# Kernel optimization log

Hardware: AMD Instinct MI355X
Metric: run time of the kernel (lower is better)

## Reference

```python
import jax, jax.numpy as jnp
import numpy as np

B, IN_DIM, D, C = 16384, 1024, 256, 100


def setup_inputs() -> dict:
    key = jax.random.key(0)
    k1, k2, k3, k4 = jax.random.split(key, 4)
    x = jax.random.normal(k1, (B, IN_DIM), dtype=jnp.float32)
    W = jax.random.normal(k2, (IN_DIM, D), dtype=jnp.float32) * (1.0 / np.sqrt(IN_DIM))
    b = jax.random.normal(k3, (D,), dtype=jnp.float32) * 0.01
    P = jax.random.normal(k4, (C, D), dtype=jnp.float32)  # class prototypes [C, D]
    return {"x": x, "W": W, "b": b, "P": P}


def reference(x, W, b, P):
    # Encoder: Z = x @ W + b  -> [B, D]
    Z = x @ W + b
    d = Z.shape[-1]
    # MSE(r, p) = mean((r - p)^2) = (|r|^2 - 2 r.p + |p|^2) / D
    # Computed via expansion to avoid the [B, C, D] broadcast intermediate.
    sq = (
        jnp.sum(Z * Z, axis=-1, keepdims=True)      # [B, 1]
        - 2.0 * (Z @ P.T)                            # [B, C]
        + jnp.sum(P * P, axis=-1)[None, :]           # [1, C]
    )
    return -sq / d  # [B, C]
```

## Files before the change

kernel.cpp:

```cpp
#include <hip/hip_runtime.h>

#define BATCH 16384
#define KDIM  1024
#define DDIM  256
#define CNUM  100
#define CPAD  112

typedef __bf16 bf16x8 __attribute__((ext_vector_type(8)));
typedef float  floatx4 __attribute__((ext_vector_type(4)));

static __device__ __forceinline__ unsigned short f2b(float f) {
    return __builtin_bit_cast(unsigned short, (__bf16)f);
}

__global__ __launch_bounds__(256) void prep(const float* __restrict__ W,
                                            const float* __restrict__ P,
                                            unsigned short* __restrict__ Wt2,
                                            unsigned short* __restrict__ Pbf,
                                            float* __restrict__ pnorm2) {
    __shared__ float T[32][33];
    const int bid = blockIdx.x;
    if (bid < 256) {
        const int k0 = (bid & 31) * 32;
        const int n0 = (bid >> 5) * 32;
        const int j  = threadIdx.x & 31;
        const int i0 = threadIdx.x >> 5;
#pragma unroll
        for (int l = 0; l < 4; ++l) {
            int i = i0 + l * 8;
            T[i][j] = W[(k0 + i) * DDIM + n0 + j];
        }
        __syncthreads();
        if (threadIdx.x < 128) {
            const int l  = threadIdx.x & 63;
            const int fn = threadIdx.x >> 6;
            const int lm = l & 15, lq = l >> 4;
            bf16x8 v;
#pragma unroll
            for (int jj = 0; jj < 8; ++jj)
                v[jj] = (__bf16)T[lq * 8 + jj][fn * 16 + lm];
            const int nblk = (n0 >> 4) + fn;
            const int kblk = k0 >> 5;
            *(bf16x8*)&Wt2[(nblk * 32 + kblk) * 512 + l * 8] = v;
        }
    } else {
        const int wave = threadIdx.x >> 6;
        const int lane = threadIdx.x & 63;
        const int c = (bid - 256) * 4 + wave;
        float s = 0.f;
#pragma unroll
        for (int jj = 0; jj < 4; ++jj) {
            int d = jj * 64 + lane;
            float v = (c < CNUM) ? P[c * DDIM + d] : 0.f;
            Pbf[c * DDIM + d] = f2b(v);
            s += v * v;
        }
#pragma unroll
        for (int m = 1; m < 64; m <<= 1) s += __shfl_xor(s, m, 64);
        if (lane == 0) pnorm2[c] = s;
    }
}

#define KSTEP(KK, CUR, NXT, P0, P1, P2, P3)                                    \
    {                                                                          \
        unsigned short* As_c = U + (CUR) * 4096;                               \
        const int kb_ = (KK) >> 5;                                             \
        if ((KK) + 64 < KDIM) {                                                \
            _Pragma("unroll")                                                  \
            for (int kf = 0; kf < 2; ++kf) {                                   \
                _Pragma("unroll")                                              \
                for (int f = 0; f < 4; ++f)                                    \
                    b[NXT][kf][f] = *(const bf16x8*)(gB + f * 16384 +          \
                                                     (kb_ + 2 + kf) * 512);    \
            }                                                                  \
            bf16x8 ha;                                                         \
            ha[0] = (__bf16)P0[0]; ha[1] = (__bf16)P0[1];                      \
            ha[2] = (__bf16)P0[2]; ha[3] = (__bf16)P0[3];                      \
            ha[4] = (__bf16)P1[0]; ha[5] = (__bf16)P1[1];                      \
            ha[6] = (__bf16)P1[2]; ha[7] = (__bf16)P1[3];                      \
            *(bf16x8*)&(U + (NXT) * 4096)[ldsA] = ha;                          \
            bf16x8 hb;                                                         \
            hb[0] = (__bf16)P2[0]; hb[1] = (__bf16)P2[1];                      \
            hb[2] = (__bf16)P2[2]; hb[3] = (__bf16)P2[3];                      \
            hb[4] = (__bf16)P3[0]; hb[5] = (__bf16)P3[1];                      \
            hb[6] = (__bf16)P3[2]; hb[7] = (__bf16)P3[3];                      \
            *(bf16x8*)&(U + (NXT) * 4096)[ldsA + 2048] = hb;                   \
            if ((KK) + 192 < KDIM) {                                           \
                P0 = *(const floatx4*)(gA + (KK) + 192);                       \
                P1 = *(const floatx4*)(gA + (KK) + 196);                       \
                P2 = *(const floatx4*)(gA2 + (KK) + 192);                      \
                P3 = *(const floatx4*)(gA2 + (KK) + 196);                      \
            }                                                                  \
        }                                                                      \
        _Pragma("unroll")                                                      \
        for (int kf = 0; kf < 2; ++kf) {                                       \
            const int sw = kf ? sw1 : sw0;                                     \
            bf16x8 a0 = *(const bf16x8*)&As_c[lm * 64 + sw];                   \
            bf16x8 a1 = *(const bf16x8*)&As_c[(16 + lm) * 64 + sw];            \
            bf16x8 a2 = *(const bf16x8*)&As_c[(32 + lm) * 64 + sw];            \
            bf16x8 a3 = *(const bf16x8*)&As_c[(48 + lm) * 64 + sw];            \
            _Pragma("unroll")                                                  \
            for (int f = 0; f < 4; ++f) {                                      \
                acc[0][f] = __builtin_amdgcn_mfma_f32_16x16x32_bf16(           \
                    a0, b[CUR][kf][f], acc[0][f], 0, 0, 0);                    \
                acc[1][f] = __builtin_amdgcn_mfma_f32_16x16x32_bf16(           \
                    a1, b[CUR][kf][f], acc[1][f], 0, 0, 0);                    \
                acc[2][f] = __builtin_amdgcn_mfma_f32_16x16x32_bf16(           \
                    a2, b[CUR][kf][f], acc[2][f], 0, 0, 0);                    \
                acc[3][f] = __builtin_amdgcn_mfma_f32_16x16x32_bf16(           \
                    a3, b[CUR][kf][f], acc[3][f], 0, 0, 0);                    \
            }                                                                  \
        }                                                                      \
        asm volatile("s_waitcnt lgkmcnt(0)\n\ts_barrier" ::: "memory");        \
    }

__global__ __launch_bounds__(256, 1) void fused_main(
    const float* __restrict__ x, const float* __restrict__ bias,
    const unsigned short* __restrict__ Wt2, const unsigned short* __restrict__ Pbf,
    const float* __restrict__ pnorm2, float* __restrict__ out)
{
    __shared__ unsigned short U[16896];
    __shared__ float rn2[4][64];
    unsigned short* Zs = U;

    const int tid  = threadIdx.x;
    const int wave = tid >> 6;
    const int lane = tid & 63;
    const int lm   = lane & 15;
    const int lq   = lane >> 4;
    const int r0   = blockIdx.x * 64;

    const int rowA = tid >> 3;
    const int kbA  = tid & 7;
    const float* gA  = x + (r0 + rowA) * KDIM + kbA * 8;
    const float* gA2 = gA + 32 * KDIM;
    const int ldsA = rowA * 64 + ((kbA ^ (rowA & 7)) * 8);

    const unsigned short* gB = Wt2 + wave * 4 * 16384 + lane * 8;

    const int sw0 = ((0 * 4 + lq) ^ (lm & 7)) * 8;
    const int sw1 = ((1 * 4 + lq) ^ (lm & 7)) * 8;

    floatx4 acc[4][4];
#pragma unroll
    for (int g = 0; g < 4; ++g)
#pragma unroll
        for (int f = 0; f < 4; ++f) { acc[g][f][0]=0.f; acc[g][f][1]=0.f; acc[g][f][2]=0.f; acc[g][f][3]=0.f; }

    bf16x8 b[2][2][4];

    {
        floatx4 q0 = *(const floatx4*)(gA);
        floatx4 q1 = *(const floatx4*)(gA + 4);
        floatx4 q2 = *(const floatx4*)(gA2);
        floatx4 q3 = *(const floatx4*)(gA2 + 4);
        bf16x8 ha;
        ha[0] = (__bf16)q0[0]; ha[1] = (__bf16)q0[1];
        ha[2] = (__bf16)q0[2]; ha[3] = (__bf16)q0[3];
        ha[4] = (__bf16)q1[0]; ha[5] = (__bf16)q1[1];
        ha[6] = (__bf16)q1[2]; ha[7] = (__bf16)q1[3];
        *(bf16x8*)&U[ldsA] = ha;
        bf16x8 hb;
        hb[0] = (__bf16)q2[0]; hb[1] = (__bf16)q2[1];
        hb[2] = (__bf16)q2[2]; hb[3] = (__bf16)q2[3];
        hb[4] = (__bf16)q3[0]; hb[5] = (__bf16)q3[1];
        hb[6] = (__bf16)q3[2]; hb[7] = (__bf16)q3[3];
        *(bf16x8*)&U[ldsA + 2048] = hb;
    }
#pragma unroll
    for (int kf = 0; kf < 2; ++kf)
#pragma unroll
        for (int f = 0; f < 4; ++f)
            b[0][kf][f] = *(const bf16x8*)(gB + f * 16384 + kf * 512);
    floatx4 pa0 = *(const floatx4*)(gA + 64);
    floatx4 pa1 = *(const floatx4*)(gA + 68);
    floatx4 pa2 = *(const floatx4*)(gA2 + 64);
    floatx4 pa3 = *(const floatx4*)(gA2 + 68);
    floatx4 pb0 = *(const floatx4*)(gA + 128);
    floatx4 pb1 = *(const floatx4*)(gA + 132);
    floatx4 pb2 = *(const floatx4*)(gA2 + 128);
    floatx4 pb3 = *(const floatx4*)(gA2 + 132);
    asm volatile("s_waitcnt lgkmcnt(0)\n\ts_barrier" ::: "memory");

    for (int kk0 = 0; kk0 < KDIM; kk0 += 128) {
        KSTEP(kk0,      0, 1, pa0, pa1, pa2, pa3)
        KSTEP(kk0 + 64, 1, 0, pb0, pb1, pb2, pb3)
    }

#pragma unroll
    for (int f = 0; f < 4; ++f) {
        float bb = bias[wave * 64 + f * 16 + lm];
#pragma unroll
        for (int g = 0; g < 4; ++g)
#pragma unroll
            for (int r = 0; r < 4; ++r) acc[g][f][r] += bb;
    }

#pragma unroll
    for (int g = 0; g < 4; ++g) {
        float s0 = 0.f, s1 = 0.f, s2 = 0.f, s3 = 0.f;
#pragma unroll
        for (int f = 0; f < 4; ++f) {
            s0 += acc[g][f][0] * acc[g][f][0];
            s1 += acc[g][f][1] * acc[g][f][1];
            s2 += acc[g][f][2] * acc[g][f][2];
            s3 += acc[g][f][3] * acc[g][f][3];
        }
#pragma unroll
        for (int m = 1; m < 16; m <<= 1) {
            s0 += __shfl_xor(s0, m, 64);
            s1 += __shfl_xor(s1, m, 64);
            s2 += __shfl_xor(s2, m, 64);
            s3 += __shfl_xor(s3, m, 64);
        }
        if (lm == 0) {
            int rl = g * 16 + lq * 4;
            rn2[wave][rl + 0] = s0;
            rn2[wave][rl + 1] = s1;
            rn2[wave][rl + 2] = s2;
            rn2[wave][rl + 3] = s3;
        }
    }

#pragma unroll
    for (int g = 0; g < 4; ++g)
#pragma unroll
        for (int f = 0; f < 4; ++f) {
            int col = wave * 64 + f * 16 + lm;
#pragma unroll
            for (int r = 0; r < 4; ++r)
                Zs[(g * 16 + lq * 4 + r) * 264 + col] = f2b(acc[g][f][r]);
        }
    __syncthreads();

#pragma unroll
    for (int t = 0; t < 2; ++t) {
        const int ct = wave * 2 + t;
        if (ct < 7) {
            floatx4 acc2[4];
#pragma unroll
            for (int nf = 0; nf < 4; ++nf) { acc2[nf][0]=0.f; acc2[nf][1]=0.f; acc2[nf][2]=0.f; acc2[nf][3]=0.f; }
            const unsigned short* gP = Pbf + (ct * 16 + lm) * DDIM + lq * 8;
#pragma unroll
            for (int ks = 0; ks < 8; ++ks) {
                bf16x8 ap = *(const bf16x8*)(gP + ks * 32);
#pragma unroll
                for (int nf = 0; nf < 4; ++nf) {
                    bf16x8 bz = *(const bf16x8*)&Zs[(nf * 16 + lm) * 264 + ks * 32 + lq * 8];
                    acc2[nf] = __builtin_amdgcn_mfma_f32_16x16x32_bf16(ap, bz, acc2[nf], 0, 0, 0);
                }
            }
            int c0 = ct * 16 + lq * 4;
            if (c0 < CNUM) {
                floatx4 pn = *(const floatx4*)(pnorm2 + c0);
#pragma unroll
                for (int nf = 0; nf < 4; ++nf) {
                    int rl = nf * 16 + lm;
                    float rn = rn2[0][rl] + rn2[1][rl] + rn2[2][rl] + rn2[3][rl];
                    floatx4 o;
#pragma unroll
                    for (int r = 0; r < 4; ++r)
                        o[r] = (2.f * acc2[nf][r] - rn - pn[r]) * (1.f / 256.f);
                    *(floatx4*)&out[(r0 + rl) * CNUM + c0] = o;
                }
            }
        }
    }
}

extern "C" void kernel_launch(void* const* d_in, const int* in_sizes, int n_in,
                              void* d_out, int out_size, void* d_ws, size_t ws_size,
                              hipStream_t stream) {
    const float* x = (const float*)d_in[0];
    const float* W = (const float*)d_in[1];
    const float* b = (const float*)d_in[2];
    const float* P = (const float*)d_in[3];
    float* out = (float*)d_out;

    unsigned short* Wt2 = (unsigned short*)d_ws;
    unsigned short* Pbf = Wt2 + KDIM * DDIM;
    float* pn2 = (float*)(Pbf + CPAD * DDIM);

    prep<<<256 + CPAD / 4, 256, 0, stream>>>(W, P, Wt2, Pbf, pn2);
    fused_main<<<BATCH / 64, 256, 0, stream>>>(x, b, Wt2, Pbf, pn2, out);
}
```

Measured before the change: 113.9 us.

## Split K across two wave groups with LDS reduction, doubling block size

```diff
diff --git a/kernel.cpp b/kernel.cpp
--- a/kernel.cpp
+++ b/kernel.cpp
@@ -5,6 +5,7 @@
 #define DDIM  256
 #define CNUM  100
 #define CPAD  112
+#define RSTR  72
 
 typedef __bf16 bf16x8 __attribute__((ext_vector_type(8)));
 typedef float  floatx4 __attribute__((ext_vector_type(4)));
@@ -63,14 +64,14 @@
 
 #define KSTEP(KK, CUR, NXT, P0, P1, P2, P3)                                    \
     {                                                                          \
-        unsigned short* As_c = U + (CUR) * 4096;                               \
+        const unsigned short* As_c = U16 + (CUR) * 8192 + kh * 4096;           \
         const int kb_ = (KK) >> 5;                                             \
-        if ((KK) + 64 < KDIM) {                                                \
+        if ((KK) + 64 < 512) {                                                 \
             _Pragma("unroll")                                                  \
             for (int kf = 0; kf < 2; ++kf) {                                   \
                 _Pragma("unroll")                                              \
                 for (int f = 0; f < 4; ++f)                                    \
-                    b[NXT][kf][f] = *(const bf16x8*)(gB + f * 16384 +          \
+                    b[NXT][kf * 4 + f] = *(const bf16x8*)(gB + f * 16384 +     \
                                                      (kb_ + 2 + kf) * 512);    \
             }                                                                  \
             bf16x8 ha;                                                         \
@@ -78,18 +79,18 @@
             ha[2] = (__bf16)P0[2]; ha[3] = (__bf16)P0[3];                      \
             ha[4] = (__bf16)P1[0]; ha[5] = (__bf16)P1[1];                      \
             ha[6] = (__bf16)P1[2]; ha[7] = (__bf16)P1[3];                      \
-            *(bf16x8*)&(U + (NXT) * 4096)[ldsA] = ha;                          \
+            *(bf16x8*)&U16[(NXT) * 8192 + ldsA] = ha;                          \
             bf16x8 hb;                                                         \
             hb[0] = (__bf16)P2[0]; hb[1] = (__bf16)P2[1];                      \
             hb[2] = (__bf16)P2[2]; hb[3] = (__bf16)P2[3];                      \
             hb[4] = (__bf16)P3[0]; hb[5] = (__bf16)P3[1];                      \
             hb[6] = (__bf16)P3[2]; hb[7] = (__bf16)P3[3];                      \
-            *(bf16x8*)&(U + (NXT) * 4096)[ldsA + 2048] = hb;                   \
-            if ((KK) + 192 < KDIM) {                                           \
+            *(bf16x8*)&U16[(NXT) * 8192 + 4096 + ldsA] = hb;                   \
+            if ((KK) + 192 < 512) {                                            \
                 P0 = *(const floatx4*)(gA + (KK) + 192);                       \
                 P1 = *(const floatx4*)(gA + (KK) + 196);                       \
-                P2 = *(const floatx4*)(gA2 + (KK) + 192);                      \
-                P3 = *(const floatx4*)(gA2 + (KK) + 196);                      \
+                P2 = *(const floatx4*)(gA + 512 + (KK) + 192);                 \
+                P3 = *(const floatx4*)(gA + 512 + (KK) + 196);                 \
             }                                                                  \
         }                                                                      \
         _Pragma("unroll")                                                      \
@@ -102,29 +103,33 @@
             _Pragma("unroll")                                                  \
             for (int f = 0; f < 4; ++f) {                                      \
                 acc[0][f] = __builtin_amdgcn_mfma_f32_16x16x32_bf16(           \
-                    a0, b[CUR][kf][f], acc[0][f], 0, 0, 0);                    \
+                    a0, b[CUR][kf * 4 + f], acc[0][f], 0, 0, 0);               \
                 acc[1][f] = __builtin_amdgcn_mfma_f32_16x16x32_bf16(           \
-                    a1, b[CUR][kf][f], acc[1][f], 0, 0, 0);                    \
+                    a1, b[CUR][kf * 4 + f], acc[1][f], 0, 0, 0);               \
                 acc[2][f] = __builtin_amdgcn_mfma_f32_16x16x32_bf16(           \
-                    a2, b[CUR][kf][f], acc[2][f], 0, 0, 0);                    \
+                    a2, b[CUR][kf * 4 + f], acc[2][f], 0, 0, 0);               \
                 acc[3][f] = __builtin_amdgcn_mfma_f32_16x16x32_bf16(           \
-                    a3, b[CUR][kf][f], acc[3][f], 0, 0, 0);                    \
+                    a3, b[CUR][kf * 4 + f], acc[3][f], 0, 0, 0);               \
             }                                                                  \
         }                                                                      \
         asm volatile("s_waitcnt lgkmcnt(0)\n\ts_barrier" ::: "memory");        \
     }
 
-__global__ __launch_bounds__(256, 1) void fused_main(
+__global__ __launch_bounds__(512, 2) void fused_main(
     const float* __restrict__ x, const float* __restrict__ bias,
     const unsigned short* __restrict__ Wt2, const unsigned short* __restrict__ Pbf,
     const float* __restrict__ pnorm2, float* __restrict__ out)
 {
-    __shared__ unsigned short U[16896];
+    __shared__ __align__(16) float Ubuf[4 * 64 * RSTR];
     __shared__ float rn2[4][64];
-    unsigned short* Zs = U;
+    unsigned short* U16 = (unsigned short*)Ubuf;
+    float* Rs = Ubuf;
+    unsigned short* Zs = (unsigned short*)Ubuf;
 
     const int tid  = threadIdx.x;
     const int wave = tid >> 6;
+    const int kh   = wave >> 2;
+    const int wn   = wave & 3;
     const int lane = tid & 63;
     const int lm   = lane & 15;
     const int lq   = lane >> 4;
@@ -132,11 +137,10 @@
 
     const int rowA = tid >> 3;
     const int kbA  = tid & 7;
-    const float* gA  = x + (r0 + rowA) * KDIM + kbA * 8;
-    const float* gA2 = gA + 32 * KDIM;
+    const float* gA = x + (size_t)(r0 + rowA) * KDIM + kbA * 8;
     const int ldsA = rowA * 64 + ((kbA ^ (rowA & 7)) * 8);
 
-    const unsigned short* gB = Wt2 + wave * 4 * 16384 + lane * 8;
+    const unsigned short* gB = Wt2 + wn * 65536 + kh * 8192 + lane * 8;
 
     const int sw0 = ((0 * 4 + lq) ^ (lm & 7)) * 8;
     const int sw1 = ((1 * 4 + lq) ^ (lm & 7)) * 8;
@@ -147,95 +151,114 @@
 #pragma unroll
         for (int f = 0; f < 4; ++f) { acc[g][f][0]=0.f; acc[g][f][1]=0.f; acc[g][f][2]=0.f; acc[g][f][3]=0.f; }
 
-    bf16x8 b[2][2][4];
+    bf16x8 b[2][8];
 
     {
         floatx4 q0 = *(const floatx4*)(gA);
         floatx4 q1 = *(const floatx4*)(gA + 4);
-        floatx4 q2 = *(const floatx4*)(gA2);
-        floatx4 q3 = *(const floatx4*)(gA2 + 4);
+        floatx4 q2 = *(const floatx4*)(gA + 512);
+        floatx4 q3 = *(const floatx4*)(gA + 516);
         bf16x8 ha;
         ha[0] = (__bf16)q0[0]; ha[1] = (__bf16)q0[1];
         ha[2] = (__bf16)q0[2]; ha[3] = (__bf16)q0[3];
         ha[4] = (__bf16)q1[0]; ha[5] = (__bf16)q1[1];
         ha[6] = (__bf16)q1[2]; ha[7] = (__bf16)q1[3];
-        *(bf16x8*)&U[ldsA] = ha;
+        *(bf16x8*)&U16[ldsA] = ha;
         bf16x8 hb;
         hb[0] = (__bf16)q2[0]; hb[1] = (__bf16)q2[1];
         hb[2] = (__bf16)q2[2]; hb[3] = (__bf16)q2[3];
         hb[4] = (__bf16)q3[0]; hb[5] = (__bf16)q3[1];
         hb[6] = (__bf16)q3[2]; hb[7] = (__bf16)q3[3];
-        *(bf16x8*)&U[ldsA + 2048] = hb;
+        *(bf16x8*)&U16[4096 + ldsA] = hb;
     }
 #pragma unroll
     for (int kf = 0; kf < 2; ++kf)
 #pragma unroll
         for (int f = 0; f < 4; ++f)
-            b[0][kf][f] = *(const bf16x8*)(gB + f * 16384 + kf * 512);
+            b[0][kf * 4 + f] = *(const bf16x8*)(gB + f * 16384 + kf * 512);
     floatx4 pa0 = *(const floatx4*)(gA + 64);
     floatx4 pa1 = *(const floatx4*)(gA + 68);
-    floatx4 pa2 = *(const floatx4*)(gA2 + 64);
-    floatx4 pa3 = *(const floatx4*)(gA2 + 68);
+    floatx4 pa2 = *(const floatx4*)(gA + 576);
+    floatx4 pa3 = *(const floatx4*)(gA + 580);
     floatx4 pb0 = *(const floatx4*)(gA + 128);
     floatx4 pb1 = *(const floatx4*)(gA + 132);
-    floatx4 pb2 = *(const floatx4*)(gA2 + 128);
-    floatx4 pb3 = *(const floatx4*)(gA2 + 132);
+    floatx4 pb2 = *(const floatx4*)(gA + 640);
+    floatx4 pb3 = *(const floatx4*)(gA + 644);
     asm volatile("s_waitcnt lgkmcnt(0)\n\ts_barrier" ::: "memory");
 
-    for (int kk0 = 0; kk0 < KDIM; kk0 += 128) {
+    for (int kk0 = 0; kk0 < 512; kk0 += 128) {
         KSTEP(kk0,      0, 1, pa0, pa1, pa2, pa3)
         KSTEP(kk0 + 64, 1, 0, pb0, pb1, pb2, pb3)
     }
 
-#pragma unroll
-    for (int f = 0; f < 4; ++f) {
-        float bb = bias[wave * 64 + f * 16 + lm];
+    if (kh == 1) {
 #pragma unroll
         for (int g = 0; g < 4; ++g)
 #pragma unroll
-            for (int r = 0; r < 4; ++r) acc[g][f][r] += bb;
-    }
-
-#pragma unroll
-    for (int g = 0; g < 4; ++g) {
-        float s0 = 0.f, s1 = 0.f, s2 = 0.f, s3 = 0.f;
+            for (int f = 0; f < 4; ++f)
+                *(floatx4*)&Rs[(wn * 64 + f * 16 + lm) * RSTR + g * 16 + lq * 4] = acc[g][f];
+    }
+    __syncthreads();
+    if (kh == 0) {
+#pragma unroll
+        for (int g = 0; g < 4; ++g)
+#pragma unroll
+            for (int f = 0; f < 4; ++f) {
+                floatx4 p = *(const floatx4*)&Rs[(wn * 64 + f * 16 + lm) * RSTR + g * 16 + lq * 4];
+#pragma unroll
+                for (int r = 0; r < 4; ++r) acc[g][f][r] += p[r];
+            }
 #pragma unroll
         for (int f = 0; f < 4; ++f) {
-            s0 += acc[g][f][0] * acc[g][f][0];
-            s1 += acc[g][f][1] * acc[g][f][1];
-            s2 += acc[g][f][2] * acc[g][f][2];
-            s3 += acc[g][f][3] * acc[g][f][3];
-        }
-#pragma unroll
-        for (int m = 1; m < 16; m <<= 1) {
-            s0 += __shfl_xor(s0, m, 64);
-            s1 += __shfl_xor(s1, m, 64);
-            s2 += __shfl_xor(s2, m, 64);
-            s3 += __shfl_xor(s3, m, 64);
-        }
-        if (lm == 0) {
-            int rl = g * 16 + lq * 4;
-            rn2[wave][rl + 0] = s0;
-            rn2[wave][rl + 1] = s1;
-            rn2[wave][rl + 2] = s2;
-            rn2[wave][rl + 3] = s3;
-        }
-    }
-
-#pragma unroll
-    for (int g = 0; g < 4; ++g)
-#pragma unroll
-        for (int f = 0; f < 4; ++f) {
-            int col = wave * 64 + f * 16 + lm;
-#pragma unroll
-            for (int r = 0; r < 4; ++r)
-                Zs[(g * 16 + lq * 4 + r) * 264 + col] = f2b(acc[g][f][r]);
-        }
+            float bb = bias[wn * 64 + f * 16 + lm];
+#pragma unroll
+            for (int g = 0; g < 4; ++g)
+#pragma unroll
+                for (int r = 0; r < 4; ++r) acc[g][f][r] += bb;
+        }
+#pragma unroll
+        for (int g = 0; g < 4; ++g) {
+            float s0 = 0.f, s1 = 0.f, s2 = 0.f, s3 = 0.f;
+#pragma unroll
+            for (int f = 0; f < 4; ++f) {
+                s0 += acc[g][f][0] * acc[g][f][0];
+                s1 += acc[g][f][1] * acc[g][f][1];
+                s2 += acc[g][f][2] * acc[g][f][2];
+                s3 += acc[g][f][3] * acc[g][f][3];
+            }
+#pragma unroll
+            for (int m = 1; m < 16; m <<= 1) {
+                s0 += __shfl_xor(s0, m, 64);
+                s1 += __shfl_xor(s1, m, 64);
+                s2 += __shfl_xor(s2, m, 64);
+                s3 += __shfl_xor(s3, m, 64);
+            }
+            if (lm == 0) {
+                int rl = g * 16 + lq * 4;
+                rn2[wn][rl + 0] = s0;
+                rn2[wn][rl + 1] = s1;
+                rn2[wn][rl + 2] = s2;
+                rn2[wn][rl + 3] = s3;
+            }
+        }
+    }
     __syncthreads();
 
-#pragma unroll
-    for (int t = 0; t < 2; ++t) {
-        const int ct = wave * 2 + t;
+    if (kh == 0) {
+#pragma unroll
+        for (int g = 0; g < 4; ++g)
+#pragma unroll
+            for (int f = 0; f < 4; ++f) {
+                int col = wn * 64 + f * 16 + lm;
+#pragma unroll
+                for (int r = 0; r < 4; ++r)
+                    Zs[(g * 16 + lq * 4 + r) * 264 + col] = f2b(acc[g][f][r]);
+            }
+    }
+    __syncthreads();
+
+    {
+        const int ct = wave;
         if (ct < 7) {
             floatx4 acc2[4];
 #pragma unroll
@@ -282,5 +305,5 @@
     float* pn2 = (float*)(Pbf + CPAD * DDIM);
 
     prep<<<256 + CPAD / 4, 256, 0, stream>>>(W, P, Wt2, Pbf, pn2);
-    fused_main<<<BATCH / 64, 256, 0, stream>>>(x, b, Wt2, Pbf, pn2, out);
+    fused_main<<<BATCH / 64, 512, 0, stream>>>(x, b, Wt2, Pbf, pn2, out);
 }
```

After: 112.1 us. No clear change (-1.6%).
